# Optimization experiments

Hardware: AMD Instinct MI355X
Metric: run time of the kernel (lower is better)

Reference implementation:

```python
import jax, jax.numpy as jnp
import numpy as np

B, S, H, L = 64, 512, 768, 3

def setup_inputs() -> dict:
    key = jax.random.key(0)
    ks = jax.random.split(key, 6)
    hidden = jax.random.normal(ks[0], (B, S, H), dtype=jnp.float32)
    attention_mask = jnp.ones((B, S), dtype=jnp.int32)
    labels = jax.random.randint(ks[1], (B, S), 0, L)
    W = jax.random.normal(ks[2], (H, L), dtype=jnp.float32) * 0.02
    b = jnp.zeros((L,), dtype=jnp.float32)
    start_transitions = jax.random.normal(ks[3], (L,), dtype=jnp.float32) * 0.1
    end_transitions = jax.random.normal(ks[4], (L,), dtype=jnp.float32) * 0.1
    transitions = jax.random.normal(ks[5], (L, L), dtype=jnp.float32) * 0.1
    return {"hidden": hidden, "W": W, "b": b,
            "start_transitions": start_transitions,
            "end_transitions": end_transitions,
            "transitions": transitions,
            "attention_mask": attention_mask, "labels": labels}

def _crf_nll(emissions, tags, mask, start_transitions, end_transitions, transitions):
    # emissions [B,S,L], tags [B,S] int, mask [B,S] float (contiguous, mask[:,0]=1)
    em_t = jnp.transpose(emissions, (1, 0, 2))   # [S,B,L]
    tags_t = tags.T                              # [S,B]
    mask_t = mask.T                              # [S,B]

    # --- gold-path score ---
    e0 = jnp.take_along_axis(em_t[0], tags_t[0][:, None], axis=1)[:, 0]
    score0 = start_transitions[tags_t[0]] + e0   # [B]

    def gold_step(carry, inp):
        score, prev_tags, last_tags = carry
        em, tg, m = inp
        e = jnp.take_along_axis(em, tg[:, None], axis=1)[:, 0]
        t = transitions[prev_tags, tg]
        score = score + (e + t) * m
        last_tags = jnp.where(m > 0, tg, last_tags)
        return (score, tg, last_tags), None

    (score, _, last_tags), _ = jax.lax.scan(
        gold_step, (score0, tags_t[0], tags_t[0]),
        (em_t[1:], tags_t[1:], mask_t[1:]))
    score = score + end_transitions[last_tags]   # [B]

    # --- log-partition via forward algorithm ---
    alpha0 = start_transitions[None, :] + em_t[0]  # [B,L]

    def fwd_step(alpha, inp):
        em, m = inp
        # [B,prev,next]: alpha + transition + next emission
        nxt = jax.nn.logsumexp(alpha[:, :, None] + transitions[None, :, :]
                               + em[:, None, :], axis=1)
        alpha = jnp.where(m[:, None] > 0, nxt, alpha)
        return alpha, None

    alpha, _ = jax.lax.scan(fwd_step, alpha0, (em_t[1:], mask_t[1:]))
    log_z = jax.nn.logsumexp(alpha + end_transitions[None, :], axis=1)  # [B]

    return -jnp.mean(score - log_z)  # reduction='mean', negated

def reference(hidden, W, b, start_transitions, end_transitions, transitions,
              attention_mask, labels):
    # classifier (dropout is identity in eval)
    emissions = hidden @ W + b                     # [B,S,L]
    crf_labels = jnp.where(labels < 0, 0, labels)  # masked_fill(labels<0, O)
    maskf = attention_mask.astype(emissions.dtype)
    loss = _crf_nll(emissions, crf_labels, maskf,
                    start_transitions, end_transitions, transitions)
    return loss
```

## Files before the change

kernel.cpp:

```cpp
#include <hip/hip_runtime.h>
#include <math.h>

#define HD 768
#define NL 3
#define BB 64
#define SS 512
#define NEG (-1e30f)

__device__ __forceinline__ float lse3(float x, float y, float z) {
    float m = fmaxf(fmaxf(x, y), z);
    return m + __logf(__expf(x - m) + __expf(y - m) + __expf(z - m));
}

__global__ __launch_bounds__(256) void emis_kernel(
    const float* __restrict__ hidden, const float* __restrict__ W,
    const float* __restrict__ bias, float* __restrict__ em,
    float* __restrict__ out) {
    if (blockIdx.x == 0 && threadIdx.x == 0) out[0] = 0.f;
    int gid  = blockIdx.x * blockDim.x + threadIdx.x;
    int wave = gid >> 6;
    int lane = threadIdx.x & 63;
    int BS = BB * SS;
    if (wave >= BS) return;
    const float4* h4 = (const float4*)(hidden + (size_t)wave * HD);
    float a0 = 0.f, a1 = 0.f, a2 = 0.f;
#pragma unroll
    for (int i = 0; i < 3; ++i) {
        int k4 = lane + 64 * i;
        float4 v = h4[k4];
        int k = k4 * 4;
        a0 = fmaf(v.x, W[(k + 0) * 3 + 0], a0);
        a1 = fmaf(v.x, W[(k + 0) * 3 + 1], a1);
        a2 = fmaf(v.x, W[(k + 0) * 3 + 2], a2);
        a0 = fmaf(v.y, W[(k + 1) * 3 + 0], a0);
        a1 = fmaf(v.y, W[(k + 1) * 3 + 1], a1);
        a2 = fmaf(v.y, W[(k + 1) * 3 + 2], a2);
        a0 = fmaf(v.z, W[(k + 2) * 3 + 0], a0);
        a1 = fmaf(v.z, W[(k + 2) * 3 + 1], a1);
        a2 = fmaf(v.z, W[(k + 2) * 3 + 2], a2);
        a0 = fmaf(v.w, W[(k + 3) * 3 + 0], a0);
        a1 = fmaf(v.w, W[(k + 3) * 3 + 1], a1);
        a2 = fmaf(v.w, W[(k + 3) * 3 + 2], a2);
    }
#pragma unroll
    for (int off = 32; off; off >>= 1) {
        a0 += __shfl_down(a0, off);
        a1 += __shfl_down(a1, off);
        a2 += __shfl_down(a2, off);
    }
    if (lane == 0) {
        int b = wave >> 9;
        int s = wave & (SS - 1);
        float* o = em + ((size_t)b * SS + s) * NL;
        o[0] = a0 + bias[0];
        o[1] = a1 + bias[1];
        o[2] = a2 + bias[2];
    }
}

__global__ __launch_bounds__(64) void crf_scan_kernel(
    const float* __restrict__ em,
    const int* __restrict__ mask,
    const int* __restrict__ labels,
    const float* __restrict__ startT, const float* __restrict__ endT,
    const float* __restrict__ trans, float* __restrict__ out) {
    int b = blockIdx.x;
    int l = threadIdx.x;

    float T00 = trans[0], T01 = trans[1], T02 = trans[2];
    float T10 = trans[3], T11 = trans[4], T12 = trans[5];
    float T20 = trans[6], T21 = trans[7], T22 = trans[8];

    const float* emb = em + (size_t)b * SS * NL;
    const int*   tg  = labels + b * SS;
    const int*   mk  = mask + b * SS;
    int s0 = l * 8;

    const float4* ep = (const float4*)(emb + (size_t)s0 * NL);
    float4 E0 = ep[0], E1 = ep[1], E2 = ep[2];
    float4 E3 = ep[3], E4 = ep[4], E5 = ep[5];
    int4 ta  = ((const int4*)(tg + s0))[0];
    int4 tb4 = ((const int4*)(tg + s0))[1];
    int4 ma  = ((const int4*)(mk + s0))[0];
    int4 mb4 = ((const int4*)(mk + s0))[1];
    int pv = (l > 0) ? tg[s0 - 1] : 0;
    int prev = pv < 0 ? 0 : pv;

    float P00, P01, P02, P10, P11, P12, P20, P21, P22;
    float gold = 0.f;
    int last_s = -1, last_t = 0;

#define GOLD(kk, ee0, ee1, ee2, tt, mm, ACT)                                   \
    int t = (tt) < 0 ? 0 : (tt);                                               \
    bool act = (ACT) && ((mm) != 0);                                           \
    {                                                                          \
        float ev = (t == 0) ? (ee0) : ((t == 1) ? (ee1) : (ee2));              \
        float r0 = (t == 0) ? T00 : ((t == 1) ? T01 : T02);                    \
        float r1 = (t == 0) ? T10 : ((t == 1) ? T11 : T12);                    \
        float r2 = (t == 0) ? T20 : ((t == 1) ? T21 : T22);                    \
        float tpt = (prev == 0) ? r0 : ((prev == 1) ? r1 : r2);                \
        gold += act ? (ev + tpt) : 0.f;                                        \
        last_t = act ? t : last_t;                                             \
        last_s = act ? (s0 + (kk)) : last_s;                                   \
        prev = t;                                                              \
    }

#define STEP0(ee0, ee1, ee2, tt, mm) {                                         \
    GOLD(0, ee0, ee1, ee2, tt, mm, (s0 > 0))                                   \
    P00 = act ? (T00 + (ee0)) : 0.f;                                           \
    P01 = act ? (T01 + (ee1)) : NEG;                                           \
    P02 = act ? (T02 + (ee2)) : NEG;                                           \
    P10 = act ? (T10 + (ee0)) : NEG;                                           \
    P11 = act ? (T11 + (ee1)) : 0.f;                                           \
    P12 = act ? (T12 + (ee2)) : NEG;                                           \
    P20 = act ? (T20 + (ee0)) : NEG;                                           \
    P21 = act ? (T21 + (ee1)) : NEG;                                           \
    P22 = act ? (T22 + (ee2)) : 0.f;                                           \
}

#define STEPK(kk, ee0, ee1, ee2, tt, mm) {                                     \
    GOLD(kk, ee0, ee1, ee2, tt, mm, true)                                      \
    float n00 = lse3(P00 + T00, P01 + T10, P02 + T20) + (ee0);                 \
    float n01 = lse3(P00 + T01, P01 + T11, P02 + T21) + (ee1);                 \
    float n02 = lse3(P00 + T02, P01 + T12, P02 + T22) + (ee2);                 \
    float n10 = lse3(P10 + T00, P11 + T10, P12 + T20) + (ee0);                 \
    float n11 = lse3(P10 + T01, P11 + T11, P12 + T21) + (ee1);                 \
    float n12 = lse3(P10 + T02, P11 + T12, P12 + T22) + (ee2);                 \
    float n20 = lse3(P20 + T00, P21 + T10, P22 + T20) + (ee0);                 \
    float n21 = lse3(P20 + T01, P21 + T11, P22 + T21) + (ee1);                 \
    float n22 = lse3(P20 + T02, P21 + T12, P22 + T22) + (ee2);                 \
    P00 = act ? n00 : P00; P01 = act ? n01 : P01; P02 = act ? n02 : P02;       \
    P10 = act ? n10 : P10; P11 = act ? n11 : P11; P12 = act ? n12 : P12;       \
    P20 = act ? n20 : P20; P21 = act ? n21 : P21; P22 = act ? n22 : P22;       \
}

    STEP0(    E0.x, E0.y, E0.z, ta.x,  ma.x)
    STEPK(1,  E0.w, E1.x, E1.y, ta.y,  ma.y)
    STEPK(2,  E1.z, E1.w, E2.x, ta.z,  ma.z)
    STEPK(3,  E2.y, E2.z, E2.w, ta.w,  ma.w)
    STEPK(4,  E3.x, E3.y, E3.z, tb4.x, mb4.x)
    STEPK(5,  E3.w, E4.x, E4.y, tb4.y, mb4.y)
    STEPK(6,  E4.z, E4.w, E5.x, tb4.z, mb4.z)
    STEPK(7,  E5.y, E5.z, E5.w, tb4.w, mb4.w)

#pragma unroll
    for (int off = 1; off < 64; off <<= 1) {
        float B00 = __shfl_down(P00, off), B01 = __shfl_down(P01, off);
        float B02 = __shfl_down(P02, off), B10 = __shfl_down(P10, off);
        float B11 = __shfl_down(P11, off), B12 = __shfl_down(P12, off);
        float B20 = __shfl_down(P20, off), B21 = __shfl_down(P21, off);
        float B22 = __shfl_down(P22, off);
        float n00 = lse3(P00 + B00, P01 + B10, P02 + B20);
        float n01 = lse3(P00 + B01, P01 + B11, P02 + B21);
        float n02 = lse3(P00 + B02, P01 + B12, P02 + B22);
        float n10 = lse3(P10 + B00, P11 + B10, P12 + B20);
        float n11 = lse3(P10 + B01, P11 + B11, P12 + B21);
        float n12 = lse3(P10 + B02, P11 + B12, P12 + B22);
        float n20 = lse3(P20 + B00, P21 + B10, P22 + B20);
        float n21 = lse3(P20 + B01, P21 + B11, P22 + B21);
        float n22 = lse3(P20 + B02, P21 + B12, P22 + B22);
        P00 = n00; P01 = n01; P02 = n02;
        P10 = n10; P11 = n11; P12 = n12;
        P20 = n20; P21 = n21; P22 = n22;

        gold += __shfl_down(gold, off);
        int os = __shfl_down(last_s, off);
        int ot = __shfl_down(last_t, off);
        if (os > last_s) { last_s = os; last_t = ot; }
    }

    if (l == 0) {
        int t0 = ta.x < 0 ? 0 : ta.x;
        float st0 = startT[0], st1 = startT[1], st2 = startT[2];
        float en0 = endT[0],   en1 = endT[1],   en2 = endT[2];
        float e00 = E0.x, e01 = E0.y, e02 = E0.z;
        float a0 = st0 + e00, a1 = st1 + e01, a2 = st2 + e02;
        float f0 = lse3(a0 + P00, a1 + P10, a2 + P20);
        float f1 = lse3(a0 + P01, a1 + P11, a2 + P21);
        float f2 = lse3(a0 + P02, a1 + P12, a2 + P22);
        float logZ = lse3(f0 + en0, f1 + en1, f2 + en2);
        float sc0 = ((t0 == 0) ? st0 : ((t0 == 1) ? st1 : st2)) +
                    ((t0 == 0) ? e00 : ((t0 == 1) ? e01 : e02));
        if (last_s < 0) last_t = t0;
        float endv = (last_t == 0) ? en0 : ((last_t == 1) ? en1 : en2);
        float score = sc0 + gold + endv;
        atomicAdd(out, (logZ - score) * (1.0f / BB));
    }
}

extern "C" void kernel_launch(void* const* d_in, const int* in_sizes, int n_in,
                              void* d_out, int out_size, void* d_ws, size_t ws_size,
                              hipStream_t stream) {
    const float* hidden = (const float*)d_in[0];
    const float* W      = (const float*)d_in[1];
    const float* bias   = (const float*)d_in[2];
    const float* startT = (const float*)d_in[3];
    const float* endT   = (const float*)d_in[4];
    const float* trans  = (const float*)d_in[5];
    const int*   mask   = (const int*)d_in[6];
    const int*   labels = (const int*)d_in[7];
    float* out = (float*)d_out;

    float* em = (float*)d_ws;

    int BS = BB * SS;
    int blocks = BS / 4;
    emis_kernel<<<blocks, 256, 0, stream>>>(hidden, W, bias, em, out);
    crf_scan_kernel<<<BB, 64, 0, stream>>>(em, mask, labels, startT, endT,
                                           trans, out);
}
```

Baseline: 30.96 us.

## Split CRF scan across four waves per sequence with LDS combine

The CRF scan kernel now uses 256 threads per batch row, so each thread handles 2 timesteps instead of 8. The four wave-level prefix products of the 3x3 log-semiring matrices are combined through shared memory by thread 0. The aim is a shorter serial chain of per-thread lse steps, traded for an extra block barrier and a serial four-way combine on one thread.

```diff
diff --git a/kernel.cpp b/kernel.cpp
--- a/kernel.cpp
+++ b/kernel.cpp
@@ -58,14 +58,16 @@
     }
 }
 
-__global__ __launch_bounds__(64) void crf_scan_kernel(
+__global__ __launch_bounds__(256) void crf_fused_kernel(
     const float* __restrict__ em,
     const int* __restrict__ mask,
     const int* __restrict__ labels,
     const float* __restrict__ startT, const float* __restrict__ endT,
     const float* __restrict__ trans, float* __restrict__ out) {
     int b = blockIdx.x;
-    int l = threadIdx.x;
+    int w = threadIdx.x >> 6;
+    int l = threadIdx.x & 63;
+    int s0 = w * 128 + l * 2;
 
     float T00 = trans[0], T01 = trans[1], T02 = trans[2];
     float T10 = trans[3], T11 = trans[4], T12 = trans[5];
@@ -74,25 +76,21 @@
     const float* emb = em + (size_t)b * SS * NL;
     const int*   tg  = labels + b * SS;
     const int*   mk  = mask + b * SS;
-    int s0 = l * 8;
-
-    const float4* ep = (const float4*)(emb + (size_t)s0 * NL);
-    float4 E0 = ep[0], E1 = ep[1], E2 = ep[2];
-    float4 E3 = ep[3], E4 = ep[4], E5 = ep[5];
-    int4 ta  = ((const int4*)(tg + s0))[0];
-    int4 tb4 = ((const int4*)(tg + s0))[1];
-    int4 ma  = ((const int4*)(mk + s0))[0];
-    int4 mb4 = ((const int4*)(mk + s0))[1];
-    int pv = (l > 0) ? tg[s0 - 1] : 0;
+
+    const float2* e2 = (const float2*)(emb + (size_t)s0 * NL);
+    float2 v01 = e2[0], v23 = e2[1], v45 = e2[2];
+    int2 tt = *(const int2*)(tg + s0);
+    int2 mm = *(const int2*)(mk + s0);
+    int pv = (s0 > 0) ? tg[s0 - 1] : 0;
     int prev = pv < 0 ? 0 : pv;
 
     float P00, P01, P02, P10, P11, P12, P20, P21, P22;
     float gold = 0.f;
     int last_s = -1, last_t = 0;
 
-#define GOLD(kk, ee0, ee1, ee2, tt, mm, ACT)                                   \
-    int t = (tt) < 0 ? 0 : (tt);                                               \
-    bool act = (ACT) && ((mm) != 0);                                           \
+#define GOLD(kk, ee0, ee1, ee2, tv, mv, ACT)                                   \
+    int t = (tv) < 0 ? 0 : (tv);                                               \
+    bool act = (ACT) && ((mv) != 0);                                           \
     {                                                                          \
         float ev = (t == 0) ? (ee0) : ((t == 1) ? (ee1) : (ee2));              \
         float r0 = (t == 0) ? T00 : ((t == 1) ? T01 : T02);                    \
@@ -105,8 +103,8 @@
         prev = t;                                                              \
     }
 
-#define STEP0(ee0, ee1, ee2, tt, mm) {                                         \
-    GOLD(0, ee0, ee1, ee2, tt, mm, (s0 > 0))                                   \
+#define STEP0(ee0, ee1, ee2, tv, mv) {                                         \
+    GOLD(0, ee0, ee1, ee2, tv, mv, (s0 > 0))                                   \
     P00 = act ? (T00 + (ee0)) : 0.f;                                           \
     P01 = act ? (T01 + (ee1)) : NEG;                                           \
     P02 = act ? (T02 + (ee2)) : NEG;                                           \
@@ -118,8 +116,8 @@
     P22 = act ? (T22 + (ee2)) : 0.f;                                           \
 }
 
-#define STEPK(kk, ee0, ee1, ee2, tt, mm) {                                     \
-    GOLD(kk, ee0, ee1, ee2, tt, mm, true)                                      \
+#define STEPK(kk, ee0, ee1, ee2, tv, mv) {                                     \
+    GOLD(kk, ee0, ee1, ee2, tv, mv, true)                                      \
     float n00 = lse3(P00 + T00, P01 + T10, P02 + T20) + (ee0);                 \
     float n01 = lse3(P00 + T01, P01 + T11, P02 + T21) + (ee1);                 \
     float n02 = lse3(P00 + T02, P01 + T12, P02 + T22) + (ee2);                 \
@@ -134,14 +132,8 @@
     P20 = act ? n20 : P20; P21 = act ? n21 : P21; P22 = act ? n22 : P22;       \
 }
 
-    STEP0(    E0.x, E0.y, E0.z, ta.x,  ma.x)
-    STEPK(1,  E0.w, E1.x, E1.y, ta.y,  ma.y)
-    STEPK(2,  E1.z, E1.w, E2.x, ta.z,  ma.z)
-    STEPK(3,  E2.y, E2.z, E2.w, ta.w,  ma.w)
-    STEPK(4,  E3.x, E3.y, E3.z, tb4.x, mb4.x)
-    STEPK(5,  E3.w, E4.x, E4.y, tb4.y, mb4.y)
-    STEPK(6,  E4.z, E4.w, E5.x, tb4.z, mb4.z)
-    STEPK(7,  E5.y, E5.z, E5.w, tb4.w, mb4.w)
+    STEP0(    v01.x, v01.y, v23.x, tt.x, mm.x)
+    STEPK(1,  v23.y, v45.x, v45.y, tt.y, mm.y)
 
 #pragma unroll
     for (int off = 1; off < 64; off <<= 1) {
@@ -169,22 +161,62 @@
         if (os > last_s) { last_s = os; last_t = ot; }
     }
 
+    __shared__ float lds[4][12];
     if (l == 0) {
-        int t0 = ta.x < 0 ? 0 : ta.x;
+        lds[w][0] = P00; lds[w][1] = P01; lds[w][2] = P02;
+        lds[w][3] = P10; lds[w][4] = P11; lds[w][5] = P12;
+        lds[w][6] = P20; lds[w][7] = P21; lds[w][8] = P22;
+        lds[w][9] = gold;
+        lds[w][10] = __int_as_float(last_s);
+        lds[w][11] = __int_as_float(last_t);
+    }
+    __syncthreads();
+
+    if (threadIdx.x == 0) {
+        float R00 = lds[0][0], R01 = lds[0][1], R02 = lds[0][2];
+        float R10 = lds[0][3], R11 = lds[0][4], R12 = lds[0][5];
+        float R20 = lds[0][6], R21 = lds[0][7], R22 = lds[0][8];
+        float g  = lds[0][9];
+        int ls = __float_as_int(lds[0][10]), lt = __float_as_int(lds[0][11]);
+#pragma unroll
+        for (int c = 1; c < 4; ++c) {
+            float B00 = lds[c][0], B01 = lds[c][1], B02 = lds[c][2];
+            float B10 = lds[c][3], B11 = lds[c][4], B12 = lds[c][5];
+            float B20 = lds[c][6], B21 = lds[c][7], B22 = lds[c][8];
+            float n00 = lse3(R00 + B00, R01 + B10, R02 + B20);
+            float n01 = lse3(R00 + B01, R01 + B11, R02 + B21);
+            float n02 = lse3(R00 + B02, R01 + B12, R02 + B22);
+            float n10 = lse3(R10 + B00, R11 + B10, R12 + B20);
+            float n11 = lse3(R10 + B01, R11 + B11, R12 + B21);
+            float n12 = lse3(R10 + B02, R11 + B12, R12 + B22);
+            float n20 = lse3(R20 + B00, R21 + B10, R22 + B20);
+            float n21 = lse3(R20 + B01, R21 + B11, R22 + B21);
+            float n22 = lse3(R20 + B02, R21 + B12, R22 + B22);
+            R00 = n00; R01 = n01; R02 = n02;
+            R10 = n10; R11 = n11; R12 = n12;
+            R20 = n20; R21 = n21; R22 = n22;
+            g += lds[c][9];
+            int os = __float_as_int(lds[c][10]);
+            int ot = __float_as_int(lds[c][11]);
+            if (os > ls) { ls = os; lt = ot; }
+        }
+
+        float e00 = emb[0], e01 = emb[1], e02 = emb[2];
+        int t0 = tg[0]; t0 = t0 < 0 ? 0 : t0;
         float st0 = startT[0], st1 = startT[1], st2 = startT[2];
         float en0 = endT[0],   en1 = endT[1],   en2 = endT[2];
-        float e00 = E0.x, e01 = E0.y, e02 = E0.z;
-        float a0 = st0 + e00, a1 = st1 + e01, a2 = st2 + e02;
-        float f0 = lse3(a0 + P00, a1 + P10, a2 + P20);
-        float f1 = lse3(a0 + P01, a1 + P11, a2 + P21);
-        float f2 = lse3(a0 + P02, a1 + P12, a2 + P22);
+
+        float al0 = st0 + e00, al1 = st1 + e01, al2 = st2 + e02;
+        float f0 = lse3(al0 + R00, al1 + R10, al2 + R20);
+        float f1 = lse3(al0 + R01, al1 + R11, al2 + R21);
+        float f2 = lse3(al0 + R02, al1 + R12, al2 + R22);
         float logZ = lse3(f0 + en0, f1 + en1, f2 + en2);
         float sc0 = ((t0 == 0) ? st0 : ((t0 == 1) ? st1 : st2)) +
                     ((t0 == 0) ? e00 : ((t0 == 1) ? e01 : e02));
-        if (last_s < 0) last_t = t0;
-        float endv = (last_t == 0) ? en0 : ((last_t == 1) ? en1 : en2);
-        float score = sc0 + gold + endv;
-        atomicAdd(out, (logZ - score) * (1.0f / BB));
+        if (ls < 0) lt = t0;
+        float endv = (lt == 0) ? en0 : ((lt == 1) ? en1 : en2);
+        float contrib = logZ - (sc0 + g + endv);
+        atomicAdd(out, contrib * (1.0f / BB));
     }
 }
 
@@ -206,6 +238,6 @@
     int BS = BB * SS;
     int blocks = BS / 4;
     emis_kernel<<<blocks, 256, 0, stream>>>(hidden, W, bias, em, out);
-    crf_scan_kernel<<<BB, 64, 0, stream>>>(em, mask, labels, startT, endT,
-                                           trans, out);
-}
+    crf_fused_kernel<<<BB, 256, 0, stream>>>(em, mask, labels, startT, endT,
+                                             trans, out);
+}
```

Measured after the change: 30.46 us. About the same (-1.6%).
